# Optimization experiments

Hardware: AMD Instinct MI355X
Metric: run time of the kernel (lower is better)

## Reference

```python
import jax, jax.numpy as jnp
import numpy as np

N_NODES = 100000
K_HOPS = 2


def _gcn_norm(edge_index, edge_weight, num_nodes, fill_value=1.0):
    # renorm trick: add self-loops with weight fill_value, then D^-1/2 A D^-1/2
    row, col = edge_index[0], edge_index[1]
    sl = jnp.arange(num_nodes, dtype=edge_index.dtype)
    row = jnp.concatenate([row, sl])
    col = jnp.concatenate([col, sl])
    w = jnp.concatenate([edge_weight, jnp.full((num_nodes,), fill_value, edge_weight.dtype)])
    deg = jax.ops.segment_sum(w, row, num_segments=num_nodes)
    dinv = jnp.where(deg > 0, jax.lax.rsqrt(deg), 0.0)
    normed_w = dinv[row] * w * dinv[col]
    return row, col, normed_w


def setup_inputs() -> dict:
    key = jax.random.key(0)
    k1, k2, k3 = jax.random.split(key, 3)
    n_edges, d, units = 1000000, 64, 64
    x = jax.random.normal(k1, (N_NODES, d), dtype=jnp.float32)
    edge_index = jax.random.randint(k2, (2, n_edges), 0, N_NODES, dtype=jnp.int32)
    edge_weight = jnp.ones((n_edges,), dtype=jnp.float32)
    kernel = jax.random.normal(k3, (d, units), dtype=jnp.float32) * (1.0 / np.sqrt(d))
    bias = jnp.zeros((units,), dtype=jnp.float32)
    return {"x": x, "edge_index": edge_index, "edge_weight": edge_weight,
            "kernel": kernel, "bias": bias}


def reference(x, edge_index, edge_weight, kernel, bias):
    # SGC: K-hop normalized sparse propagation, then single dense linear
    row, col, w = _gcn_norm(edge_index, edge_weight, N_NODES, fill_value=1.0)
    h = x
    for _ in range(K_HOPS):
        h = jax.ops.segment_sum(w[:, None] * h[col], row, num_segments=N_NODES)
    out = h @ kernel + bias  # activation=None
    return out
```

## Files before the change

### kernel.cpp

```cpp
#include <hip/hip_runtime.h>


constexpr int kN = 100000;
constexpr int kD = 64;
constexpr int BSHIFT = 9;
constexpr int NBUCK = (kN + 511) >> BSHIFT;
constexpr int CHUNK = 4096;
constexpr int XW_ROWS = 128;

__device__ __forceinline__ float bf2f(unsigned short u) {
    return __uint_as_float(((unsigned)u) << 16);
}
__device__ __forceinline__ unsigned short f2bf(float f) {
    unsigned b = __float_as_uint(f);
    b += 0x7FFF + ((b >> 16) & 1);
    return (unsigned short)(b >> 16);
}

__global__ __launch_bounds__(256) void kA_count(const int* __restrict__ row,
                                                int* __restrict__ bc, int nblk, int E) {
    __shared__ int hist[256];
    int t = threadIdx.x;
    hist[t] = 0;
    __syncthreads();
    int g0 = blockIdx.x * CHUNK;
    int n = min(CHUNK, E - g0);
    for (int i = t; i < n; i += 256) {
        atomicAdd(&hist[row[g0 + i] >> BSHIFT], 1);
    }
    __syncthreads();
    if (t < NBUCK) bc[t * nblk + blockIdx.x] = hist[t];
}

__global__ __launch_bounds__(256) void kA_scanB(int* __restrict__ bc,
                                                int* __restrict__ tot, int nblk) {
    __shared__ int sh[256];
    int b = blockIdx.x;
    int t = threadIdx.x;
    int* p = bc + (size_t)b * nblk;
    int ipt = (nblk + 255) >> 8;
    int s0 = t * ipt;
    int s1 = min(s0 + ipt, nblk);
    int lsum = 0;
    for (int k = s0; k < s1; ++k) lsum += p[k];
    sh[t] = lsum;
    __syncthreads();
    for (int off = 1; off < 256; off <<= 1) {
        int add = (t >= off) ? sh[t - off] : 0;
        __syncthreads();
        sh[t] += add;
        __syncthreads();
    }
    int run = sh[t] - lsum;
    for (int k = s0; k < s1; ++k) {
        int v = p[k];
        p[k] = run;
        run += v;
    }
    if (t == 255) tot[b] = sh[255];
}

__global__ __launch_bounds__(256) void kA_scanT(const int* __restrict__ tot,
                                                int* __restrict__ base) {
    __shared__ int sh[256];
    int t = threadIdx.x;
    int v = (t < NBUCK) ? tot[t] : 0;
    sh[t] = v;
    __syncthreads();
    for (int off = 1; off < 256; off <<= 1) {
        int add = (t >= off) ? sh[t - off] : 0;
        __syncthreads();
        sh[t] += add;
        __syncthreads();
    }
    if (t < NBUCK) base[t] = sh[t] - v;
}

__global__ __launch_bounds__(256) void kA_place(const int* __restrict__ row,
                                                const int* __restrict__ col,
                                                const float* __restrict__ w,
                                                const int* __restrict__ bc,
                                                const int* __restrict__ base, int nblk,
                                                int2* __restrict__ tmp, int E) {
    __shared__ int hist[256];
    __shared__ int lbase[256];
    __shared__ int gb[256];
    __shared__ int cur[256];
    __shared__ int2 stage[CHUNK];
    __shared__ unsigned char bkt[CHUNK];
    int t = threadIdx.x;
    hist[t] = 0;
    __syncthreads();
    int g0 = blockIdx.x * CHUNK;
    int n = min(CHUNK, E - g0);
    for (int i = t; i < n; i += 256) {
        atomicAdd(&hist[row[g0 + i] >> BSHIFT], 1);
    }
    __syncthreads();
    int v = hist[t];
    lbase[t] = v;
    __syncthreads();
    for (int off = 1; off < 256; off <<= 1) {
        int add = (t >= off) ? lbase[t - off] : 0;
        __syncthreads();
        lbase[t] += add;
        __syncthreads();
    }
    int excl = lbase[t] - v;
    __syncthreads();
    lbase[t] = excl;
    cur[t] = excl;
    if (t < NBUCK) gb[t] = base[t] + bc[t * nblk + blockIdx.x];
    __syncthreads();
    for (int i = t; i < n; i += 256) {
        int r = row[g0 + i];
        int c = col[g0 + i];
        float wv = w[g0 + i];
        int b = r >> BSHIFT;
        int lp = atomicAdd(&cur[b], 1);
        stage[lp] = make_int2(c | ((r & 511) << 17), __float_as_int(wv));
        bkt[lp] = (unsigned char)b;
    }
    __syncthreads();
    for (int i = t; i < n; i += 256) {
        int b = bkt[i];
        tmp[gb[b] + (i - lbase[b])] = stage[i];
    }
}

__global__ __launch_bounds__(512) void kD_deg(const int2* __restrict__ tmp,
                                              const int* __restrict__ base,
                                              float* __restrict__ dinv, int E) {
    __shared__ float degs[512];
    int b = blockIdx.x;
    int t = threadIdx.x;
    degs[t] = 0.0f;
    __syncthreads();
    int gbase = base[b];
    int gend = (b == NBUCK - 1) ? E : base[b + 1];
    int node0 = b << BSHIFT;
    int nloc = min(512, kN - node0);
    for (int i = gbase + t; i < gend; i += 512) {
        int2 e = tmp[i];
        atomicAdd(&degs[(e.x >> 17) & 511], __int_as_float(e.y));
    }
    __syncthreads();
    if (t < nloc) {
        float d = 1.0f + degs[t];
        dinv[node0 + t] = (d > 0.0f) ? rsqrtf(d) : 0.0f;
    }
}

__global__ __launch_bounds__(512) void kB_sort(const int2* __restrict__ tmp,
                                               const int* __restrict__ base,
                                               const float* __restrict__ dinv,
                                               int2* __restrict__ ecw,
                                               int* __restrict__ start, int E) {
    __shared__ int hist[512];
    __shared__ int cur[512];
    int b = blockIdx.x;
    int t = threadIdx.x;
    int gbase = base[b];
    int gend = (b == NBUCK - 1) ? E : base[b + 1];
    int size = gend - gbase;
    int node0 = b << BSHIFT;
    int nloc = min(512, kN - node0);
    hist[t] = 0;
    __syncthreads();
    for (int i = t; i < size; i += 512) {
        atomicAdd(&hist[(tmp[gbase + i].x >> 17) & 511], 1);
    }
    __syncthreads();
    int v = hist[t];
    hist[t] = v;
    __syncthreads();
    for (int off = 1; off < 512; off <<= 1) {
        int add = (t >= off) ? hist[t - off] : 0;
        __syncthreads();
        hist[t] += add;
        __syncthreads();
    }
    int excl = hist[t] - v;
    __syncthreads();
    cur[t] = excl;
    __syncthreads();
    if (t < nloc) start[node0 + t] = gbase + excl;
    if (b == 0 && t == 0) start[kN] = E;
    for (int i = t; i < size; i += 512) {
        int2 e = tmp[gbase + i];
        int c = e.x & 0x1FFFF;
        int rl = (e.x >> 17) & 511;
        float wn = dinv[node0 + rl] * __int_as_float(e.y) * dinv[c];
        int lp = atomicAdd(&cur[rl], 1);
        ecw[gbase + lp] = make_int2(c << 7, __float_as_int(wn));
    }
}

__global__ __launch_bounds__(256) void k_xw(const float* __restrict__ x,
                                            const float* __restrict__ W,
                                            unsigned short* __restrict__ y, int n) {
    __shared__ float Xs[XW_ROWS][kD];
    int t = threadIdx.x;
    int lane = t & 63;
    int wv = t >> 6;
    int row0 = blockIdx.x * XW_ROWS;
    float Wc[kD];
#pragma unroll
    for (int k = 0; k < kD; ++k) Wc[k] = W[k * kD + lane];
    for (int i = t; i < XW_ROWS * (kD / 4); i += 256) {
        int r = i >> 4;
        int q = i & 15;
        float4 v = make_float4(0.0f, 0.0f, 0.0f, 0.0f);
        if (row0 + r < n)
            v = *reinterpret_cast<const float4*>(x + (size_t)(row0 + r) * kD + q * 4);
        *reinterpret_cast<float4*>(&Xs[r][q * 4]) = v;
    }
    __syncthreads();
    int rbase = wv * 32;
#pragma unroll
    for (int rr = 0; rr < 32; rr += 2) {
        int r0 = rbase + rr;
        float acc0 = 0.0f, acc1 = 0.0f;
#pragma unroll
        for (int q = 0; q < 16; ++q) {
            float4 a = *reinterpret_cast<const float4*>(&Xs[r0][q * 4]);
            float4 b = *reinterpret_cast<const float4*>(&Xs[r0 + 1][q * 4]);
            acc0 = fmaf(a.x, Wc[q * 4 + 0], acc0);
            acc1 = fmaf(b.x, Wc[q * 4 + 0], acc1);
            acc0 = fmaf(a.y, Wc[q * 4 + 1], acc0);
            acc1 = fmaf(b.y, Wc[q * 4 + 1], acc1);
            acc0 = fmaf(a.z, Wc[q * 4 + 2], acc0);
            acc1 = fmaf(b.z, Wc[q * 4 + 2], acc1);
            acc0 = fmaf(a.w, Wc[q * 4 + 3], acc0);
            acc1 = fmaf(b.w, Wc[q * 4 + 3], acc1);
        }
        int gr = row0 + r0;
        if (gr < n) y[(size_t)gr * kD + lane] = f2bf(acc0);
        if (gr + 1 < n) y[(size_t)(gr + 1) * kD + lane] = f2bf(acc1);
    }
}

template <typename OutWriter>
__device__ __forceinline__ void hop_body(const int* __restrict__ start,
                                         const int2* __restrict__ ecw,
                                         const float* __restrict__ dinv,
                                         const unsigned short* __restrict__ h_in,
                                         int n, OutWriter writeout) {
    int wv = threadIdx.x >> 6;
    int lane = threadIdx.x & 63;
    int half = lane >> 5;
    int sub = lane & 31;
    int node = blockIdx.x * 8 + wv * 2 + half;
    bool valid = node < n;
    int nd = valid ? node : (n - 1);
    const char* hb = (const char*)h_in;
    int lo = sub << 2;
    float di = dinv[nd];
    unsigned su = *(const unsigned*)(hb + ((size_t)nd << 7) + lo);
    float d2 = di * di;
    float acc0 = d2 * __uint_as_float(su << 16);
    float acc1 = d2 * __uint_as_float(su & 0xffff0000u);
    int s = start[nd], e = start[nd + 1];
    int d = e - s;
    int dmax = max(d, __shfl_xor(d, 32));
    int em1 = max(e - 1, 0);
    for (int it = 0; it < dmax; it += 4) {
        int j = s + it;
        int2 v0 = ecw[min(j + 0, em1)];
        int2 v1 = ecw[min(j + 1, em1)];
        int2 v2 = ecw[min(j + 2, em1)];
        int2 v3 = ecw[min(j + 3, em1)];
        unsigned g0 = *(const unsigned*)(hb + (unsigned)(v0.x + lo));
        unsigned g1 = *(const unsigned*)(hb + (unsigned)(v1.x + lo));
        unsigned g2 = *(const unsigned*)(hb + (unsigned)(v2.x + lo));
        unsigned g3 = *(const unsigned*)(hb + (unsigned)(v3.x + lo));
        float w0 = (it + 0 < d) ? __int_as_float(v0.y) : 0.0f;
        float w1 = (it + 1 < d) ? __int_as_float(v1.y) : 0.0f;
        float w2 = (it + 2 < d) ? __int_as_float(v2.y) : 0.0f;
        float w3 = (it + 3 < d) ? __int_as_float(v3.y) : 0.0f;
        acc0 = fmaf(w0, __uint_as_float(g0 << 16), acc0);
        acc1 = fmaf(w0, __uint_as_float(g0 & 0xffff0000u), acc1);
        acc0 = fmaf(w1, __uint_as_float(g1 << 16), acc0);
        acc1 = fmaf(w1, __uint_as_float(g1 & 0xffff0000u), acc1);
        acc0 = fmaf(w2, __uint_as_float(g2 << 16), acc0);
        acc1 = fmaf(w2, __uint_as_float(g2 & 0xffff0000u), acc1);
        acc0 = fmaf(w3, __uint_as_float(g3 << 16), acc0);
        acc1 = fmaf(w3, __uint_as_float(g3 & 0xffff0000u), acc1);
    }
    if (valid) writeout(node, sub, acc0, acc1);
}

__global__ __launch_bounds__(256) void k_hop1(const int* __restrict__ start,
                                              const int2* __restrict__ ecw,
                                              const float* __restrict__ dinv,
                                              const unsigned short* __restrict__ h_in,
                                              unsigned* __restrict__ h_out32, int n) {
    hop_body(start, ecw, dinv, h_in, n,
             [=](int node, int sub, float a0, float a1) {
                 unsigned p = (unsigned)f2bf(a0) | ((unsigned)f2bf(a1) << 16);
                 h_out32[((size_t)node << 5) + sub] = p;
             });
}

__global__ __launch_bounds__(256) void k_hop2(const int* __restrict__ start,
                                              const int2* __restrict__ ecw,
                                              const float* __restrict__ dinv,
                                              const unsigned short* __restrict__ h_in,
                                              const float* __restrict__ bias,
                                              float* __restrict__ out, int n) {
    hop_body(start, ecw, dinv, h_in, n,
             [=](int node, int sub, float a0, float a1) {
                 float2 b = *reinterpret_cast<const float2*>(bias + 2 * sub);
                 float2 o = make_float2(a0 + b.x, a1 + b.y);
                 *reinterpret_cast<float2*>(out + ((size_t)node << 6) + 2 * sub) = o;
             });
}

extern "C" void kernel_launch(void* const* d_in, const int* in_sizes, int n_in,
                              void* d_out, int out_size, void* d_ws, size_t ws_size,
                              hipStream_t stream) {
    const float* x    = (const float*)d_in[0];
    const int*   ei   = (const int*)d_in[1];
    const float* ew   = (const float*)d_in[2];
    const float* W    = (const float*)d_in[3];
    const float* bias = (const float*)d_in[4];
    const int E = in_sizes[1] / 2;
    const int* row = ei;
    const int* col = ei + E;

    const int nblk = (E + CHUNK - 1) / CHUNK;

    char* ws = (char*)d_ws;
    auto alloc = [&](size_t bytes) {
        char* p = ws;
        ws += ((bytes + 1023) & ~(size_t)1023);
        return p;
    };
    int*            base  = (int*)alloc(sizeof(int) * 256);
    int*            tot   = (int*)alloc(sizeof(int) * 256);
    int*            bc    = (int*)alloc(sizeof(int) * (size_t)NBUCK * nblk);
    int*            start = (int*)alloc(sizeof(int) * (kN + 1));
    float*          dinv  = (float*)alloc(sizeof(float) * kN);
    int2*           ecw   = (int2*)alloc(sizeof(int2) * (size_t)E);
    unsigned short* y     = (unsigned short*)alloc(sizeof(short) * (size_t)kN * kD);
    unsigned short* h1    = (unsigned short*)alloc(sizeof(short) * (size_t)kN * kD);
    int2*           tmp   = (int2*)h1;

    k_xw<<<(kN + XW_ROWS - 1) / XW_ROWS, 256, 0, stream>>>(x, W, y, kN);

    kA_count<<<nblk, 256, 0, stream>>>(row, bc, nblk, E);
    kA_scanB<<<NBUCK, 256, 0, stream>>>(bc, tot, nblk);
    kA_scanT<<<1, 256, 0, stream>>>(tot, base);
    kA_place<<<nblk, 256, 0, stream>>>(row, col, ew, bc, base, nblk, tmp, E);
    kD_deg<<<NBUCK, 512, 0, stream>>>(tmp, base, dinv, E);
    kB_sort<<<NBUCK, 512, 0, stream>>>(tmp, base, dinv, ecw, start, E);

    k_hop1<<<(kN + 7) / 8, 256, 0, stream>>>(start, ecw, dinv, y,
                                             (unsigned*)h1, kN);
    k_hop2<<<(kN + 7) / 8, 256, 0, stream>>>(start, ecw, dinv, h1, bias,
                                             (float*)d_out, kN);
}
```

Measured before the change: 141.7 us.

## Use 16 lanes per node in hops, fuse XW with row count, pad edge array

The hop kernels now assign 16 lanes per node with 8-byte (4 bf16) gathers instead of 32 lanes with 4-byte gathers, so each wave processes four nodes and issues wider loads. The edge list is padded with zeroed entries so the per-edge clamps on ecw indices can be dropped. The dense X·W kernel and the row bucket-count kernel are merged into one launch with block-index dispatch, removing one launch. Wider per-lane gathers raise register use, and the padded reads beyond a node's edge range depend on the zero padding being written each call.

```diff
diff --git a/kernel.cpp b/kernel.cpp
--- a/kernel.cpp
+++ b/kernel.cpp
@@ -7,6 +7,7 @@
 constexpr int NBUCK = (kN + 511) >> BSHIFT;
 constexpr int CHUNK = 4096;
 constexpr int XW_ROWS = 128;
+constexpr int ECW_PAD = 256;
 
 __device__ __forceinline__ float bf2f(unsigned short u) {
     return __uint_as_float(((unsigned)u) << 16);
@@ -17,193 +18,32 @@
     return (unsigned short)(b >> 16);
 }
 
-__global__ __launch_bounds__(256) void kA_count(const int* __restrict__ row,
-                                                int* __restrict__ bc, int nblk, int E) {
-    __shared__ int hist[256];
-    int t = threadIdx.x;
-    hist[t] = 0;
-    __syncthreads();
-    int g0 = blockIdx.x * CHUNK;
-    int n = min(CHUNK, E - g0);
-    for (int i = t; i < n; i += 256) {
-        atomicAdd(&hist[row[g0 + i] >> BSHIFT], 1);
-    }
-    __syncthreads();
-    if (t < NBUCK) bc[t * nblk + blockIdx.x] = hist[t];
-}
-
-__global__ __launch_bounds__(256) void kA_scanB(int* __restrict__ bc,
-                                                int* __restrict__ tot, int nblk) {
-    __shared__ int sh[256];
-    int b = blockIdx.x;
-    int t = threadIdx.x;
-    int* p = bc + (size_t)b * nblk;
-    int ipt = (nblk + 255) >> 8;
-    int s0 = t * ipt;
-    int s1 = min(s0 + ipt, nblk);
-    int lsum = 0;
-    for (int k = s0; k < s1; ++k) lsum += p[k];
-    sh[t] = lsum;
-    __syncthreads();
-    for (int off = 1; off < 256; off <<= 1) {
-        int add = (t >= off) ? sh[t - off] : 0;
-        __syncthreads();
-        sh[t] += add;
-        __syncthreads();
-    }
-    int run = sh[t] - lsum;
-    for (int k = s0; k < s1; ++k) {
-        int v = p[k];
-        p[k] = run;
-        run += v;
-    }
-    if (t == 255) tot[b] = sh[255];
-}
-
-__global__ __launch_bounds__(256) void kA_scanT(const int* __restrict__ tot,
-                                                int* __restrict__ base) {
-    __shared__ int sh[256];
-    int t = threadIdx.x;
-    int v = (t < NBUCK) ? tot[t] : 0;
-    sh[t] = v;
-    __syncthreads();
-    for (int off = 1; off < 256; off <<= 1) {
-        int add = (t >= off) ? sh[t - off] : 0;
-        __syncthreads();
-        sh[t] += add;
-        __syncthreads();
-    }
-    if (t < NBUCK) base[t] = sh[t] - v;
-}
-
-__global__ __launch_bounds__(256) void kA_place(const int* __restrict__ row,
-                                                const int* __restrict__ col,
-                                                const float* __restrict__ w,
-                                                const int* __restrict__ bc,
-                                                const int* __restrict__ base, int nblk,
-                                                int2* __restrict__ tmp, int E) {
-    __shared__ int hist[256];
-    __shared__ int lbase[256];
-    __shared__ int gb[256];
-    __shared__ int cur[256];
-    __shared__ int2 stage[CHUNK];
-    __shared__ unsigned char bkt[CHUNK];
-    int t = threadIdx.x;
-    hist[t] = 0;
-    __syncthreads();
-    int g0 = blockIdx.x * CHUNK;
-    int n = min(CHUNK, E - g0);
-    for (int i = t; i < n; i += 256) {
-        atomicAdd(&hist[row[g0 + i] >> BSHIFT], 1);
-    }
-    __syncthreads();
-    int v = hist[t];
-    lbase[t] = v;
-    __syncthreads();
-    for (int off = 1; off < 256; off <<= 1) {
-        int add = (t >= off) ? lbase[t - off] : 0;
-        __syncthreads();
-        lbase[t] += add;
-        __syncthreads();
-    }
-    int excl = lbase[t] - v;
-    __syncthreads();
-    lbase[t] = excl;
-    cur[t] = excl;
-    if (t < NBUCK) gb[t] = base[t] + bc[t * nblk + blockIdx.x];
-    __syncthreads();
-    for (int i = t; i < n; i += 256) {
-        int r = row[g0 + i];
-        int c = col[g0 + i];
-        float wv = w[g0 + i];
-        int b = r >> BSHIFT;
-        int lp = atomicAdd(&cur[b], 1);
-        stage[lp] = make_int2(c | ((r & 511) << 17), __float_as_int(wv));
-        bkt[lp] = (unsigned char)b;
-    }
-    __syncthreads();
-    for (int i = t; i < n; i += 256) {
-        int b = bkt[i];
-        tmp[gb[b] + (i - lbase[b])] = stage[i];
-    }
-}
-
-__global__ __launch_bounds__(512) void kD_deg(const int2* __restrict__ tmp,
-                                              const int* __restrict__ base,
-                                              float* __restrict__ dinv, int E) {
-    __shared__ float degs[512];
-    int b = blockIdx.x;
-    int t = threadIdx.x;
-    degs[t] = 0.0f;
-    __syncthreads();
-    int gbase = base[b];
-    int gend = (b == NBUCK - 1) ? E : base[b + 1];
-    int node0 = b << BSHIFT;
-    int nloc = min(512, kN - node0);
-    for (int i = gbase + t; i < gend; i += 512) {
-        int2 e = tmp[i];
-        atomicAdd(&degs[(e.x >> 17) & 511], __int_as_float(e.y));
-    }
-    __syncthreads();
-    if (t < nloc) {
-        float d = 1.0f + degs[t];
-        dinv[node0 + t] = (d > 0.0f) ? rsqrtf(d) : 0.0f;
-    }
-}
-
-__global__ __launch_bounds__(512) void kB_sort(const int2* __restrict__ tmp,
-                                               const int* __restrict__ base,
-                                               const float* __restrict__ dinv,
-                                               int2* __restrict__ ecw,
-                                               int* __restrict__ start, int E) {
-    __shared__ int hist[512];
-    __shared__ int cur[512];
-    int b = blockIdx.x;
-    int t = threadIdx.x;
-    int gbase = base[b];
-    int gend = (b == NBUCK - 1) ? E : base[b + 1];
-    int size = gend - gbase;
-    int node0 = b << BSHIFT;
-    int nloc = min(512, kN - node0);
-    hist[t] = 0;
-    __syncthreads();
-    for (int i = t; i < size; i += 512) {
-        atomicAdd(&hist[(tmp[gbase + i].x >> 17) & 511], 1);
-    }
-    __syncthreads();
-    int v = hist[t];
-    hist[t] = v;
-    __syncthreads();
-    for (int off = 1; off < 512; off <<= 1) {
-        int add = (t >= off) ? hist[t - off] : 0;
-        __syncthreads();
-        hist[t] += add;
-        __syncthreads();
-    }
-    int excl = hist[t] - v;
-    __syncthreads();
-    cur[t] = excl;
-    __syncthreads();
-    if (t < nloc) start[node0 + t] = gbase + excl;
-    if (b == 0 && t == 0) start[kN] = E;
-    for (int i = t; i < size; i += 512) {
-        int2 e = tmp[gbase + i];
-        int c = e.x & 0x1FFFF;
-        int rl = (e.x >> 17) & 511;
-        float wn = dinv[node0 + rl] * __int_as_float(e.y) * dinv[c];
-        int lp = atomicAdd(&cur[rl], 1);
-        ecw[gbase + lp] = make_int2(c << 7, __float_as_int(wn));
-    }
-}
-
-__global__ __launch_bounds__(256) void k_xw(const float* __restrict__ x,
-                                            const float* __restrict__ W,
-                                            unsigned short* __restrict__ y, int n) {
+__global__ __launch_bounds__(256) void k_xw_count(const float* __restrict__ x,
+                                                  const float* __restrict__ W,
+                                                  unsigned short* __restrict__ y,
+                                                  const int* __restrict__ row,
+                                                  int* __restrict__ bc,
+                                                  int nxw, int nblk, int n, int E) {
     __shared__ float Xs[XW_ROWS][kD];
-    int t = threadIdx.x;
+    int bid = blockIdx.x;
+    int t = threadIdx.x;
+    if (bid >= nxw) {
+        int cb = bid - nxw;
+        int* hist = (int*)&Xs[0][0];
+        hist[t] = 0;
+        __syncthreads();
+        int g0 = cb * CHUNK;
+        int nn = min(CHUNK, E - g0);
+        for (int i = t; i < nn; i += 256) {
+            atomicAdd(&hist[row[g0 + i] >> BSHIFT], 1);
+        }
+        __syncthreads();
+        if (t < NBUCK) bc[t * nblk + cb] = hist[t];
+        return;
+    }
     int lane = t & 63;
     int wv = t >> 6;
-    int row0 = blockIdx.x * XW_ROWS;
+    int row0 = bid * XW_ROWS;
     float Wc[kD];
 #pragma unroll
     for (int k = 0; k < kD; ++k) Wc[k] = W[k * kD + lane];
@@ -240,6 +80,172 @@
     }
 }
 
+__global__ __launch_bounds__(256) void kA_scanB(int* __restrict__ bc,
+                                                int* __restrict__ tot, int nblk) {
+    __shared__ int sh[256];
+    int b = blockIdx.x;
+    int t = threadIdx.x;
+    int* p = bc + (size_t)b * nblk;
+    int ipt = (nblk + 255) >> 8;
+    int s0 = t * ipt;
+    int s1 = min(s0 + ipt, nblk);
+    int lsum = 0;
+    for (int k = s0; k < s1; ++k) lsum += p[k];
+    sh[t] = lsum;
+    __syncthreads();
+    for (int off = 1; off < 256; off <<= 1) {
+        int add = (t >= off) ? sh[t - off] : 0;
+        __syncthreads();
+        sh[t] += add;
+        __syncthreads();
+    }
+    int run = sh[t] - lsum;
+    for (int k = s0; k < s1; ++k) {
+        int v = p[k];
+        p[k] = run;
+        run += v;
+    }
+    if (t == 255) tot[b] = sh[255];
+}
+
+__global__ __launch_bounds__(256) void kA_scanT(const int* __restrict__ tot,
+                                                int* __restrict__ base,
+                                                int2* __restrict__ ecw_pad) {
+    __shared__ int sh[256];
+    int t = threadIdx.x;
+    int v = (t < NBUCK) ? tot[t] : 0;
+    sh[t] = v;
+    __syncthreads();
+    for (int off = 1; off < 256; off <<= 1) {
+        int add = (t >= off) ? sh[t - off] : 0;
+        __syncthreads();
+        sh[t] += add;
+        __syncthreads();
+    }
+    if (t < NBUCK) base[t] = sh[t] - v;
+    ecw_pad[t] = make_int2(0, 0);
+}
+
+__global__ __launch_bounds__(256) void kA_place(const int* __restrict__ row,
+                                                const int* __restrict__ col,
+                                                const float* __restrict__ w,
+                                                const int* __restrict__ bc,
+                                                const int* __restrict__ base, int nblk,
+                                                int2* __restrict__ tmp, int E) {
+    __shared__ int hist[256];
+    __shared__ int lbase[256];
+    __shared__ int gb[256];
+    __shared__ int cur[256];
+    __shared__ int2 stage[CHUNK];
+    __shared__ unsigned char bkt[CHUNK];
+    int t = threadIdx.x;
+    hist[t] = 0;
+    __syncthreads();
+    int g0 = blockIdx.x * CHUNK;
+    int n = min(CHUNK, E - g0);
+    for (int i = t; i < n; i += 256) {
+        atomicAdd(&hist[row[g0 + i] >> BSHIFT], 1);
+    }
+    __syncthreads();
+    int v = hist[t];
+    lbase[t] = v;
+    __syncthreads();
+    for (int off = 1; off < 256; off <<= 1) {
+        int add = (t >= off) ? lbase[t - off] : 0;
+        __syncthreads();
+        lbase[t] += add;
+        __syncthreads();
+    }
+    int excl = lbase[t] - v;
+    __syncthreads();
+    lbase[t] = excl;
+    cur[t] = excl;
+    if (t < NBUCK) gb[t] = base[t] + bc[t * nblk + blockIdx.x];
+    __syncthreads();
+    for (int i = t; i < n; i += 256) {
+        int r = row[g0 + i];
+        int c = col[g0 + i];
+        float wv = w[g0 + i];
+        int b = r >> BSHIFT;
+        int lp = atomicAdd(&cur[b], 1);
+        stage[lp] = make_int2(c | ((r & 511) << 17), __float_as_int(wv));
+        bkt[lp] = (unsigned char)b;
+    }
+    __syncthreads();
+    for (int i = t; i < n; i += 256) {
+        int b = bkt[i];
+        tmp[gb[b] + (i - lbase[b])] = stage[i];
+    }
+}
+
+__global__ __launch_bounds__(512) void kD_deg(const int2* __restrict__ tmp,
+                                              const int* __restrict__ base,
+                                              float* __restrict__ dinv, int E) {
+    __shared__ float degs[512];
+    int b = blockIdx.x;
+    int t = threadIdx.x;
+    degs[t] = 0.0f;
+    __syncthreads();
+    int gbase = base[b];
+    int gend = (b == NBUCK - 1) ? E : base[b + 1];
+    int node0 = b << BSHIFT;
+    int nloc = min(512, kN - node0);
+    for (int i = gbase + t; i < gend; i += 512) {
+        int2 e = tmp[i];
+        atomicAdd(&degs[(e.x >> 17) & 511], __int_as_float(e.y));
+    }
+    __syncthreads();
+    if (t < nloc) {
+        float d = 1.0f + degs[t];
+        dinv[node0 + t] = (d > 0.0f) ? rsqrtf(d) : 0.0f;
+    }
+}
+
+__global__ __launch_bounds__(512) void kB_sort(const int2* __restrict__ tmp,
+                                               const int* __restrict__ base,
+                                               const float* __restrict__ dinv,
+                                               int2* __restrict__ ecw,
+                                               int* __restrict__ start, int E) {
+    __shared__ int hist[512];
+    __shared__ int cur[512];
+    int b = blockIdx.x;
+    int t = threadIdx.x;
+    int gbase = base[b];
+    int gend = (b == NBUCK - 1) ? E : base[b + 1];
+    int size = gend - gbase;
+    int node0 = b << BSHIFT;
+    int nloc = min(512, kN - node0);
+    hist[t] = 0;
+    __syncthreads();
+    for (int i = t; i < size; i += 512) {
+        atomicAdd(&hist[(tmp[gbase + i].x >> 17) & 511], 1);
+    }
+    __syncthreads();
+    int v = hist[t];
+    hist[t] = v;
+    __syncthreads();
+    for (int off = 1; off < 512; off <<= 1) {
+        int add = (t >= off) ? hist[t - off] : 0;
+        __syncthreads();
+        hist[t] += add;
+        __syncthreads();
+    }
+    int excl = hist[t] - v;
+    __syncthreads();
+    cur[t] = excl;
+    __syncthreads();
+    if (t < nloc) start[node0 + t] = gbase + excl;
+    if (b == 0 && t == 0) start[kN] = E;
+    for (int i = t; i < size; i += 512) {
+        int2 e = tmp[gbase + i];
+        int c = e.x & 0x1FFFF;
+        int rl = (e.x >> 17) & 511;
+        float wn = dinv[node0 + rl] * __int_as_float(e.y) * dinv[c];
+        int lp = atomicAdd(&cur[rl], 1);
+        ecw[gbase + lp] = make_int2(c << 7, __float_as_int(wn));
+    }
+}
+
 template <typename OutWriter>
 __device__ __forceinline__ void hop_body(const int* __restrict__ start,
                                          const int2* __restrict__ ecw,
@@ -248,57 +254,69 @@
                                          int n, OutWriter writeout) {
     int wv = threadIdx.x >> 6;
     int lane = threadIdx.x & 63;
-    int half = lane >> 5;
-    int sub = lane & 31;
-    int node = blockIdx.x * 8 + wv * 2 + half;
+    int q = lane >> 4;
+    int f = lane & 15;
+    int node = blockIdx.x * 16 + wv * 4 + q;
     bool valid = node < n;
     int nd = valid ? node : (n - 1);
     const char* hb = (const char*)h_in;
-    int lo = sub << 2;
+    int lo = f << 3;
     float di = dinv[nd];
-    unsigned su = *(const unsigned*)(hb + ((size_t)nd << 7) + lo);
     float d2 = di * di;
-    float acc0 = d2 * __uint_as_float(su << 16);
-    float acc1 = d2 * __uint_as_float(su & 0xffff0000u);
+    uint2 su = *(const uint2*)(hb + ((size_t)nd << 7) + lo);
+    float acc0 = d2 * __uint_as_float(su.x << 16);
+    float acc1 = d2 * __uint_as_float(su.x & 0xffff0000u);
+    float acc2 = d2 * __uint_as_float(su.y << 16);
+    float acc3 = d2 * __uint_as_float(su.y & 0xffff0000u);
     int s = start[nd], e = start[nd + 1];
     int d = e - s;
-    int dmax = max(d, __shfl_xor(d, 32));
-    int em1 = max(e - 1, 0);
+    int m1 = max(d, __shfl_xor(d, 16));
+    int dmax = max(m1, __shfl_xor(m1, 32));
     for (int it = 0; it < dmax; it += 4) {
         int j = s + it;
-        int2 v0 = ecw[min(j + 0, em1)];
-        int2 v1 = ecw[min(j + 1, em1)];
-        int2 v2 = ecw[min(j + 2, em1)];
-        int2 v3 = ecw[min(j + 3, em1)];
-        unsigned g0 = *(const unsigned*)(hb + (unsigned)(v0.x + lo));
-        unsigned g1 = *(const unsigned*)(hb + (unsigned)(v1.x + lo));
-        unsigned g2 = *(const unsigned*)(hb + (unsigned)(v2.x + lo));
-        unsigned g3 = *(const unsigned*)(hb + (unsigned)(v3.x + lo));
+        int2 v0 = ecw[j + 0];
+        int2 v1 = ecw[j + 1];
+        int2 v2 = ecw[j + 2];
+        int2 v3 = ecw[j + 3];
+        uint2 g0 = *(const uint2*)(hb + (unsigned)(v0.x + lo));
+        uint2 g1 = *(const uint2*)(hb + (unsigned)(v1.x + lo));
+        uint2 g2 = *(const uint2*)(hb + (unsigned)(v2.x + lo));
+        uint2 g3 = *(const uint2*)(hb + (unsigned)(v3.x + lo));
         float w0 = (it + 0 < d) ? __int_as_float(v0.y) : 0.0f;
         float w1 = (it + 1 < d) ? __int_as_float(v1.y) : 0.0f;
         float w2 = (it + 2 < d) ? __int_as_float(v2.y) : 0.0f;
         float w3 = (it + 3 < d) ? __int_as_float(v3.y) : 0.0f;
-        acc0 = fmaf(w0, __uint_as_float(g0 << 16), acc0);
-        acc1 = fmaf(w0, __uint_as_float(g0 & 0xffff0000u), acc1);
-        acc0 = fmaf(w1, __uint_as_float(g1 << 16), acc0);
-        acc1 = fmaf(w1, __uint_as_float(g1 & 0xffff0000u), acc1);
-        acc0 = fmaf(w2, __uint_as_float(g2 << 16), acc0);
-        acc1 = fmaf(w2, __uint_as_float(g2 & 0xffff0000u), acc1);
-        acc0 = fmaf(w3, __uint_as_float(g3 << 16), acc0);
-        acc1 = fmaf(w3, __uint_as_float(g3 & 0xffff0000u), acc1);
-    }
-    if (valid) writeout(node, sub, acc0, acc1);
+        acc0 = fmaf(w0, __uint_as_float(g0.x << 16), acc0);
+        acc1 = fmaf(w0, __uint_as_float(g0.x & 0xffff0000u), acc1);
+        acc2 = fmaf(w0, __uint_as_float(g0.y << 16), acc2);
+        acc3 = fmaf(w0, __uint_as_float(g0.y & 0xffff0000u), acc3);
+        acc0 = fmaf(w1, __uint_as_float(g1.x << 16), acc0);
+        acc1 = fmaf(w1, __uint_as_float(g1.x & 0xffff0000u), acc1);
+        acc2 = fmaf(w1, __uint_as_float(g1.y << 16), acc2);
+        acc3 = fmaf(w1, __uint_as_float(g1.y & 0xffff0000u), acc3);
+        acc0 = fmaf(w2, __uint_as_float(g2.x << 16), acc0);
+        acc1 = fmaf(w2, __uint_as_float(g2.x & 0xffff0000u), acc1);
+        acc2 = fmaf(w2, __uint_as_float(g2.y << 16), acc2);
+        acc3 = fmaf(w2, __uint_as_float(g2.y & 0xffff0000u), acc3);
+        acc0 = fmaf(w3, __uint_as_float(g3.x << 16), acc0);
+        acc1 = fmaf(w3, __uint_as_float(g3.x & 0xffff0000u), acc1);
+        acc2 = fmaf(w3, __uint_as_float(g3.y << 16), acc2);
+        acc3 = fmaf(w3, __uint_as_float(g3.y & 0xffff0000u), acc3);
+    }
+    if (valid) writeout(node, f, acc0, acc1, acc2, acc3);
 }
 
 __global__ __launch_bounds__(256) void k_hop1(const int* __restrict__ start,
                                               const int2* __restrict__ ecw,
                                               const float* __restrict__ dinv,
                                               const unsigned short* __restrict__ h_in,
-                                              unsigned* __restrict__ h_out32, int n) {
+                                              uint2* __restrict__ h_out64, int n) {
     hop_body(start, ecw, dinv, h_in, n,
-             [=](int node, int sub, float a0, float a1) {
-                 unsigned p = (unsigned)f2bf(a0) | ((unsigned)f2bf(a1) << 16);
-                 h_out32[((size_t)node << 5) + sub] = p;
+             [=](int node, int f, float a0, float a1, float a2, float a3) {
+                 uint2 p;
+                 p.x = (unsigned)f2bf(a0) | ((unsigned)f2bf(a1) << 16);
+                 p.y = (unsigned)f2bf(a2) | ((unsigned)f2bf(a3) << 16);
+                 h_out64[((size_t)node << 4) + f] = p;
              });
 }
 
@@ -309,10 +327,10 @@
                                               const float* __restrict__ bias,
                                               float* __restrict__ out, int n) {
     hop_body(start, ecw, dinv, h_in, n,
-             [=](int node, int sub, float a0, float a1) {
-                 float2 b = *reinterpret_cast<const float2*>(bias + 2 * sub);
-                 float2 o = make_float2(a0 + b.x, a1 + b.y);
-                 *reinterpret_cast<float2*>(out + ((size_t)node << 6) + 2 * sub) = o;
+             [=](int node, int f, float a0, float a1, float a2, float a3) {
+                 float4 b = *reinterpret_cast<const float4*>(bias + (f << 2));
+                 float4 o = make_float4(a0 + b.x, a1 + b.y, a2 + b.z, a3 + b.w);
+                 *reinterpret_cast<float4*>(out + ((size_t)node << 6) + (f << 2)) = o;
              });
 }
 
@@ -329,6 +347,7 @@
     const int* col = ei + E;
 
     const int nblk = (E + CHUNK - 1) / CHUNK;
+    const int nxw  = (kN + XW_ROWS - 1) / XW_ROWS;
 
     char* ws = (char*)d_ws;
     auto alloc = [&](size_t bytes) {
@@ -341,22 +360,21 @@
     int*            bc    = (int*)alloc(sizeof(int) * (size_t)NBUCK * nblk);
     int*            start = (int*)alloc(sizeof(int) * (kN + 1));
     float*          dinv  = (float*)alloc(sizeof(float) * kN);
-    int2*           ecw   = (int2*)alloc(sizeof(int2) * (size_t)E);
+    int2*           ecw   = (int2*)alloc(sizeof(int2) * (size_t)(E + ECW_PAD));
     unsigned short* y     = (unsigned short*)alloc(sizeof(short) * (size_t)kN * kD);
     unsigned short* h1    = (unsigned short*)alloc(sizeof(short) * (size_t)kN * kD);
     int2*           tmp   = (int2*)h1;
 
-    k_xw<<<(kN + XW_ROWS - 1) / XW_ROWS, 256, 0, stream>>>(x, W, y, kN);
-
-    kA_count<<<nblk, 256, 0, stream>>>(row, bc, nblk, E);
+    k_xw_count<<<nxw + nblk, 256, 0, stream>>>(x, W, y, row, bc, nxw, nblk, kN, E);
+
     kA_scanB<<<NBUCK, 256, 0, stream>>>(bc, tot, nblk);
-    kA_scanT<<<1, 256, 0, stream>>>(tot, base);
+    kA_scanT<<<1, 256, 0, stream>>>(tot, base, ecw + E);
     kA_place<<<nblk, 256, 0, stream>>>(row, col, ew, bc, base, nblk, tmp, E);
     kD_deg<<<NBUCK, 512, 0, stream>>>(tmp, base, dinv, E);
     kB_sort<<<NBUCK, 512, 0, stream>>>(tmp, base, dinv, ecw, start, E);
 
-    k_hop1<<<(kN + 7) / 8, 256, 0, stream>>>(start, ecw, dinv, y,
-                                             (unsigned*)h1, kN);
-    k_hop2<<<(kN + 7) / 8, 256, 0, stream>>>(start, ecw, dinv, h1, bias,
-                                             (float*)d_out, kN);
-}
+    k_hop1<<<(kN + 15) / 16, 256, 0, stream>>>(start, ecw, dinv, y,
+                                               (uint2*)h1, kN);
+    k_hop2<<<(kN + 15) / 16, 256, 0, stream>>>(start, ecw, dinv, h1, bias,
+                                               (float*)d_out, kN);
+}
```

Result: faster. 123.1 us, median of 2 (-13.1%).
